# Kernel optimization log

Hardware: AMD Instinct MI355X
Metric: run time of the kernel (lower is better)

## Reference

```python
import jax, jax.numpy as jnp
import numpy as np

B, IN_FEATURES, OUT_FEATURES, N_BASIS = 65536, 128, 16, 16
WEIGHT_MAGNITUDE = 1.0


def chebyshev_basis(x, n):
    # x: [B, IN] in [-1, 1] -> T_k(x) stacked: [B, IN, n]
    Ts = [jnp.ones_like(x), x]
    for _ in range(n - 2):
        Ts.append(2.0 * x * Ts[-1] - Ts[-2])
    return jnp.stack(Ts[:n], axis=-1)


def setup_inputs() -> dict:
    key = jax.random.key(0)
    k1, k2 = jax.random.split(key)
    # inputs assumed normalized to [-1, 1] (polynomial basis domain)
    x = jax.random.uniform(k1, (B, IN_FEATURES), jnp.float32, -1.0, 1.0)
    wm = WEIGHT_MAGNITUDE / IN_FEATURES
    w = jax.random.uniform(k2, (OUT_FEATURES, IN_FEATURES, N_BASIS), jnp.float32, -wm, wm)
    return {"x": x, "w": w}


def reference(x, w):
    # basis expansion [B, IN, N] contracted against w [OUT, IN, N] -> [B, OUT]
    basis = chebyshev_basis(x, w.shape[-1])
    return jnp.einsum('bin,oin->bo', basis, w)
```

## Files before the change

kernel.cpp:

```cpp
#include <hip/hip_runtime.h>
#include <hip/hip_bf16.h>

typedef _Float16 f16x8 __attribute__((ext_vector_type(8)));
typedef __fp16  fp16x2 __attribute__((ext_vector_type(2)));
typedef float f32x4 __attribute__((ext_vector_type(4)));

#define IN_F 128
#define OUT_F 16
#define NB 16

__global__ void prep_w_kernel(const float* __restrict__ w, _Float16* __restrict__ wf) {
    int qi = blockIdx.x * 256 + threadIdx.x;
    int n = qi & 15;
    int f = (qi >> 4) & 127;
    int o = qi >> 11;
    int P = f >> 4, rem = f & 15, g = rem >> 2, q = rem & 3;
    int h = n >> 3, j = n & 7;
    int ks = 8 * P + 2 * q + h;
    int l = g * 16 + o;
    wf[(ks * 64 + l) * 8 + j] = (_Float16)w[qi];
}

__device__ __forceinline__ void cheb_frags(float xv, f16x8& ae, f16x8& ao) {
    float x2 = xv + xv;
    float t2  = __builtin_fmaf(x2, xv,  -1.0f);
    float t3  = __builtin_fmaf(x2, t2,  -xv);
    float t4  = __builtin_fmaf(x2, t3,  -t2);
    float t5  = __builtin_fmaf(x2, t4,  -t3);
    float t6  = __builtin_fmaf(x2, t5,  -t4);
    float t7  = __builtin_fmaf(x2, t6,  -t5);
    float t8  = __builtin_fmaf(x2, t7,  -t6);
    float t9  = __builtin_fmaf(x2, t8,  -t7);
    float t10 = __builtin_fmaf(x2, t9,  -t8);
    float t11 = __builtin_fmaf(x2, t10, -t9);
    float t12 = __builtin_fmaf(x2, t11, -t10);
    float t13 = __builtin_fmaf(x2, t12, -t11);
    float t14 = __builtin_fmaf(x2, t13, -t12);
    float t15 = __builtin_fmaf(x2, t14, -t13);
    union { f16x8 v; fp16x2 h[4]; } e, od;
    e.h[0]  = __builtin_amdgcn_cvt_pkrtz(1.0f, xv);
    e.h[1]  = __builtin_amdgcn_cvt_pkrtz(t2,  t3);
    e.h[2]  = __builtin_amdgcn_cvt_pkrtz(t4,  t5);
    e.h[3]  = __builtin_amdgcn_cvt_pkrtz(t6,  t7);
    od.h[0] = __builtin_amdgcn_cvt_pkrtz(t8,  t9);
    od.h[1] = __builtin_amdgcn_cvt_pkrtz(t10, t11);
    od.h[2] = __builtin_amdgcn_cvt_pkrtz(t12, t13);
    od.h[3] = __builtin_amdgcn_cvt_pkrtz(t14, t15);
    ae = e.v;
    ao = od.v;
}

__global__ __launch_bounds__(256) void cheb_main(const float* __restrict__ x,
                                                 const _Float16* __restrict__ wf,
                                                 float* __restrict__ out) {
    const int tid = threadIdx.x;
    const long row0 = (long)blockIdx.x * 128;

    const int l  = tid & 63;
    const int wv = tid >> 6;
    const int g  = l >> 4;
    const int o  = l & 15;
    const int lm = l & 15;

    const long r0 = row0 + wv * 32 + lm;
    const long r1 = r0 + 16;

    const f32x4* x4 = (const f32x4*)x;
    const f16x8* wfv = (const f16x8*)wf;

    f32x4 acc0 = {0.f, 0.f, 0.f, 0.f};
    f32x4 acc1 = {0.f, 0.f, 0.f, 0.f};

    #pragma unroll
    for (int P = 0; P < 8; ++P) {
        f32x4 xv0 = x4[r0 * 32 + P * 4 + g];
        f32x4 xv1 = x4[r1 * 32 + P * 4 + g];
        #pragma unroll
        for (int q = 0; q < 4; ++q) {
            int ks = 8 * P + 2 * q;
            f16x8 b0 = wfv[ks * 64 + l];
            f16x8 b1 = wfv[ks * 64 + 64 + l];
            f16x8 a0e, a0o, a1e, a1o;
            cheb_frags(xv0[q], a0e, a0o);
            cheb_frags(xv1[q], a1e, a1o);
            acc0 = __builtin_amdgcn_mfma_f32_16x16x32_f16(a0e, b0, acc0, 0, 0, 0);
            acc0 = __builtin_amdgcn_mfma_f32_16x16x32_f16(a0o, b1, acc0, 0, 0, 0);
            acc1 = __builtin_amdgcn_mfma_f32_16x16x32_f16(a1e, b0, acc1, 0, 0, 0);
            acc1 = __builtin_amdgcn_mfma_f32_16x16x32_f16(a1o, b1, acc1, 0, 0, 0);
        }
    }

    float* op = out + (row0 + wv * 32 + 4 * g) * OUT_F + o;
    #pragma unroll
    for (int rr = 0; rr < 4; ++rr) {
        op[rr * OUT_F] = acc0[rr];
        op[(16 + rr) * OUT_F] = acc1[rr];
    }
}

extern "C" void kernel_launch(void* const* d_in, const int* in_sizes, int n_in,
                              void* d_out, int out_size, void* d_ws, size_t ws_size,
                              hipStream_t stream) {
    const float* x = (const float*)d_in[0];
    const float* w = (const float*)d_in[1];
    float* out = (float*)d_out;
    _Float16* wf = (_Float16*)d_ws;

    prep_w_kernel<<<128, 256, 0, stream>>>(w, wf);
    cheb_main<<<512, 256, 0, stream>>>(x, wf, out);
}
```

Before: 19.70 us.

## Fuse weight fp16 conversion into main kernel via swizzled LDS staging

Removes the separate weight-prep kernel launch. Each block now converts the fp32 weights to fp16 itself and stages them in a 64KB XOR-swizzled LDS buffer, and the MFMA loop reads its B fragments from LDS instead of global memory. All x values are prefetched into registers before the weight staging. The cost is redundant per-block conversion of 128KB of weights, a barrier, large LDS use that limits occupancy, and higher register pressure.

```diff
diff --git a/kernel.cpp b/kernel.cpp
--- a/kernel.cpp
+++ b/kernel.cpp
@@ -8,18 +8,6 @@
 #define IN_F 128
 #define OUT_F 16
 #define NB 16
-
-__global__ void prep_w_kernel(const float* __restrict__ w, _Float16* __restrict__ wf) {
-    int qi = blockIdx.x * 256 + threadIdx.x;
-    int n = qi & 15;
-    int f = (qi >> 4) & 127;
-    int o = qi >> 11;
-    int P = f >> 4, rem = f & 15, g = rem >> 2, q = rem & 3;
-    int h = n >> 3, j = n & 7;
-    int ks = 8 * P + 2 * q + h;
-    int l = g * 16 + o;
-    wf[(ks * 64 + l) * 8 + j] = (_Float16)w[qi];
-}
 
 __device__ __forceinline__ void cheb_frags(float xv, f16x8& ae, f16x8& ao) {
     float x2 = xv + xv;
@@ -50,9 +38,10 @@
     ao = od.v;
 }
 
-__global__ __launch_bounds__(256) void cheb_main(const float* __restrict__ x,
-                                                 const _Float16* __restrict__ wf,
-                                                 float* __restrict__ out) {
+__global__ __launch_bounds__(256) void cheb_fused(const float* __restrict__ x,
+                                                  const float* __restrict__ w,
+                                                  float* __restrict__ out) {
+    __shared__ _Float16 wlds[32768];
     const int tid = threadIdx.x;
     const long row0 = (long)blockIdx.x * 128;
 
@@ -64,25 +53,51 @@
 
     const long r0 = row0 + wv * 32 + lm;
     const long r1 = r0 + 16;
+    const f32x4* x4 = (const f32x4*)x;
 
-    const f32x4* x4 = (const f32x4*)x;
-    const f16x8* wfv = (const f16x8*)wf;
+    f32x4 xa[8], xb[8];
+    #pragma unroll
+    for (int P = 0; P < 8; ++P) {
+        xa[P] = x4[r0 * 32 + P * 4 + g];
+        xb[P] = x4[r1 * 32 + P * 4 + g];
+    }
+
+    #pragma unroll
+    for (int k = 0; k < 8; ++k) {
+        int p = k * 256 + tid;
+        const float4* src = (const float4*)(w + (size_t)p * 16);
+        float4 a = src[0], b = src[1], c = src[2], d = src[3];
+        union { f16x8 v; fp16x2 h[4]; } E, O;
+        E.h[0] = __builtin_amdgcn_cvt_pkrtz(a.x, a.y);
+        E.h[1] = __builtin_amdgcn_cvt_pkrtz(a.z, a.w);
+        E.h[2] = __builtin_amdgcn_cvt_pkrtz(b.x, b.y);
+        E.h[3] = __builtin_amdgcn_cvt_pkrtz(b.z, b.w);
+        O.h[0] = __builtin_amdgcn_cvt_pkrtz(c.x, c.y);
+        O.h[1] = __builtin_amdgcn_cvt_pkrtz(c.z, c.w);
+        O.h[2] = __builtin_amdgcn_cvt_pkrtz(d.x, d.y);
+        O.h[3] = __builtin_amdgcn_cvt_pkrtz(d.z, d.w);
+        int s0 = (2 * p) ^ ((p >> 7) & 7);
+        *(f16x8*)&wlds[s0 * 8]       = E.v;
+        *(f16x8*)&wlds[(s0 ^ 1) * 8] = O.v;
+    }
+    __syncthreads();
 
     f32x4 acc0 = {0.f, 0.f, 0.f, 0.f};
     f32x4 acc1 = {0.f, 0.f, 0.f, 0.f};
 
+    const int Aslot = 256 * o + 8 * g;
+    const int key = o & 7;
+
     #pragma unroll
     for (int P = 0; P < 8; ++P) {
-        f32x4 xv0 = x4[r0 * 32 + P * 4 + g];
-        f32x4 xv1 = x4[r1 * 32 + P * 4 + g];
         #pragma unroll
         for (int q = 0; q < 4; ++q) {
-            int ks = 8 * P + 2 * q;
-            f16x8 b0 = wfv[ks * 64 + l];
-            f16x8 b1 = wfv[ks * 64 + 64 + l];
+            int s0 = Aslot + 32 * P + ((2 * q) ^ key);
+            f16x8 b0 = *(const f16x8*)&wlds[s0 * 8];
+            f16x8 b1 = *(const f16x8*)&wlds[(s0 ^ 1) * 8];
             f16x8 a0e, a0o, a1e, a1o;
-            cheb_frags(xv0[q], a0e, a0o);
-            cheb_frags(xv1[q], a1e, a1o);
+            cheb_frags(xa[P][q], a0e, a0o);
+            cheb_frags(xb[P][q], a1e, a1o);
             acc0 = __builtin_amdgcn_mfma_f32_16x16x32_f16(a0e, b0, acc0, 0, 0, 0);
             acc0 = __builtin_amdgcn_mfma_f32_16x16x32_f16(a0o, b1, acc0, 0, 0, 0);
             acc1 = __builtin_amdgcn_mfma_f32_16x16x32_f16(a1e, b0, acc1, 0, 0, 0);
@@ -104,8 +119,5 @@
     const float* x = (const float*)d_in[0];
     const float* w = (const float*)d_in[1];
     float* out = (float*)d_out;
-    _Float16* wf = (_Float16*)d_ws;
-
-    prep_w_kernel<<<128, 256, 0, stream>>>(w, wf);
-    cheb_main<<<512, 256, 0, stream>>>(x, wf, out);
+    cheb_fused<<<512, 256, 0, stream>>>(x, w, out);
 }
```

Result: faster. 17.88 us (-9.2%).
